# Optimization experiments

Hardware: AMD Instinct MI355X
Metric: run time of the kernel (lower is better)

## Reference

```python
import jax, jax.numpy as jnp
import numpy as np

N_EXPERTS = 8
TOP_K = 2
AUX_COEF = 0.01
Z_COEF = 0.001


def setup_inputs() -> dict:
    key = jax.random.key(0)
    ks = jax.random.split(key, 5)
    B, S, D, F, E = 2, 2048, 768, 2048, N_EXPERTS
    std = 0.02
    std_out = std / np.sqrt(2 * 12)  # scale_init_by_depth, n_layers=12
    return {
        "x": jax.random.normal(ks[0], (B, S, D), jnp.float32),
        "router_w": jax.random.normal(ks[1], (D, E), jnp.float32) * std,
        "w1": jax.random.normal(ks[2], (E, D, F), jnp.float32) * std,
        "w2": jax.random.normal(ks[3], (E, F, D), jnp.float32) * std_out,
        "w3": jax.random.normal(ks[4], (E, D, F), jnp.float32) * std,
    }


def reference(x, router_w, w1, w2, w3):
    B, S, D = x.shape
    E = w1.shape[0]
    x_flat = x.reshape(-1, D)                      # [N, D]
    n_tokens = x_flat.shape[0]

    router_logits = x_flat @ router_w               # [N, E]
    probs = jax.nn.softmax(router_logits.astype(jnp.float32), axis=-1)
    topk_w, topk_i = jax.lax.top_k(probs, TOP_K)    # [N, K]
    topk_w = topk_w / jnp.sum(topk_w, axis=-1, keepdims=True)

    # Combine: equivalent to sort/group dispatch + per-expert GEMM + index_add,
    # expressed as a masked per-expert (fixed, small E) dense pass.
    out = jnp.zeros((n_tokens, D), dtype=x.dtype)
    for e in range(E):
        gate = jnp.sum(jnp.where(topk_i == e, topk_w, 0.0), axis=-1)  # [N] f32
        h = jax.nn.silu(x_flat @ w1[e]) * (x_flat @ w3[e])            # [N, F]
        out = out + gate[:, None].astype(x.dtype) * (h @ w2[e])

    # Switch-style load-balancing aux loss + z-loss
    importance = probs.mean(axis=0)                 # [E]
    top1 = topk_i[:, 0]
    load = jnp.zeros((E,), jnp.float32).at[top1].add(1.0) / n_tokens
    aux_loss = E * jnp.sum(importance * load) * AUX_COEF
    z_loss = jnp.mean(router_logits.astype(jnp.float32) ** 2) * Z_COEF

    return out.reshape(B, S, D), aux_loss, z_loss
```

## Files before the change

### kernel.cpp

```cpp
#include <hip/hip_runtime.h>
#include <hip/hip_bf16.h>

constexpr int NT = 4096;
constexpr int DD = 768;
constexpr int FF = 2048;
constexpr int NE = 8;
constexpr int MAXROWS = 9216;
constexpr int MAXMT128 = 72;
constexpr int MAXMT256 = 40;
constexpr int NKT1 = DD / 64;

constexpr int IDX_CNTA   = 0;
constexpr int IDX_CNTT1  = 8;
constexpr int IDX_CUR    = 16;
constexpr int IDX_IMP    = 24;
constexpr int IDX_ZSUM   = 32;
constexpr int IDX_NTILES = 33;
constexpr int IDX_OFF    = 34;
constexpr int IDX_EXPT   = 48;
constexpr int IDX_N256   = 120;
constexpr int IDX_E256   = 128;
constexpr int IDX_B256   = 168;
constexpr int IDX_L256   = 208;

constexpr size_t OFF_META   = 0;
constexpr size_t OFF_TKE    = 1024;
constexpr size_t OFF_GATE   = OFF_TKE    + (size_t)NT*2*4;
constexpr size_t OFF_ROWOF  = OFF_GATE   + (size_t)NT*2*4;
constexpr size_t OFF_TOKROW = OFF_ROWOF  + (size_t)NT*2*4;
constexpr size_t OFF_XG     = 136192;
constexpr size_t OFF_W1T    = OFF_XG  + (size_t)MAXROWS*DD*2;
constexpr size_t OFF_W3T    = OFF_W1T + (size_t)NE*FF*DD*2;
constexpr size_t OFF_W2T    = OFF_W3T + (size_t)NE*FF*DD*2;
constexpr size_t OFF_H      = OFF_W2T + (size_t)NE*FF*DD*2;
constexpr size_t OFF_OP     = OFF_H   + (size_t)MAXROWS*FF*2;

typedef float f32x4 __attribute__((ext_vector_type(4)));
typedef __bf16 bf16x8v __attribute__((ext_vector_type(8)));
typedef unsigned short u16x8 __attribute__((ext_vector_type(8)));

__device__ inline unsigned short f2bf_bits(float f) {
  __bf16 h = (__bf16)f;
  return *(unsigned short*)&h;
}
__device__ inline float bf2f(unsigned short u) {
  unsigned v = (unsigned)u << 16;
  return *(float*)&v;
}

__device__ __forceinline__ void glds16(const void* g, void* l) {
  __builtin_amdgcn_global_load_lds(
      (const __attribute__((address_space(1))) unsigned int*)g,
      (__attribute__((address_space(3))) unsigned int*)l, 16, 0, 0);
}

constexpr int RB = 128;
__global__ __launch_bounds__(256) void router_kernel(const float* __restrict__ x,
    const float* __restrict__ rw, int* __restrict__ meta,
    int* __restrict__ tke, float* __restrict__ gateArr) {
  __shared__ float s_imp[NE];
  __shared__ float s_z;
  __shared__ int s_cnt1[NE], s_cnta[NE];
  if (threadIdx.x < NE) { s_imp[threadIdx.x] = 0.f; s_cnt1[threadIdx.x] = 0; s_cnta[threadIdx.x] = 0; }
  if (threadIdx.x == 0) s_z = 0.f;
  __syncthreads();

  const int wave = threadIdx.x >> 6, lane = threadIdx.x & 63;
  float impacc[NE];
  #pragma unroll
  for (int e = 0; e < NE; ++e) impacc[e] = 0.f;
  float zacc = 0.f;

  for (int t = blockIdx.x * 4 + wave; t < NT; t += RB * 4) {
    float acc[NE];
    #pragma unroll
    for (int e = 0; e < NE; ++e) acc[e] = 0.f;
    const float* xr = x + (size_t)t * DD;
    for (int i = lane; i < DD; i += 64) {
      float xv = xr[i];
      const float* r = rw + i * NE;
      #pragma unroll
      for (int e = 0; e < NE; ++e) acc[e] += xv * r[e];
    }
    #pragma unroll
    for (int off = 32; off > 0; off >>= 1) {
      #pragma unroll
      for (int e = 0; e < NE; ++e) acc[e] += __shfl_xor(acc[e], off);
    }
    float mx = acc[0];
    #pragma unroll
    for (int e = 1; e < NE; ++e) mx = fmaxf(mx, acc[e]);
    float p[NE]; float s = 0.f;
    #pragma unroll
    for (int e = 0; e < NE; ++e) { p[e] = __expf(acc[e] - mx); s += p[e]; }
    float inv = 1.f / s;
    #pragma unroll
    for (int e = 0; e < NE; ++e) p[e] *= inv;
    int e0 = 0; float p0 = p[0];
    #pragma unroll
    for (int e = 1; e < NE; ++e) if (p[e] > p0) { p0 = p[e]; e0 = e; }
    int e1 = -1; float p1 = -1.f;
    #pragma unroll
    for (int e = 0; e < NE; ++e) if (e != e0 && p[e] > p1) { p1 = p[e]; e1 = e; }
    if (lane == 0) {
      #pragma unroll
      for (int e = 0; e < NE; ++e) { impacc[e] += p[e]; zacc += acc[e] * acc[e]; }
      atomicAdd(&s_cnt1[e0], 1);
      atomicAdd(&s_cnta[e0], 1);
      atomicAdd(&s_cnta[e1], 1);
      float gs = 1.f / (p0 + p1);
      tke[t*2]   = e0; tke[t*2+1] = e1;
      gateArr[t*2] = p0 * gs; gateArr[t*2+1] = p1 * gs;
    }
  }
  if (lane == 0) {
    #pragma unroll
    for (int e = 0; e < NE; ++e) atomicAdd(&s_imp[e], impacc[e]);
    atomicAdd(&s_z, zacc);
  }
  __syncthreads();
  float* fmeta = (float*)meta;
  if (threadIdx.x < NE) {
    atomicAdd(&fmeta[IDX_IMP + threadIdx.x], s_imp[threadIdx.x]);
    atomicAdd(&meta[IDX_CNTT1 + threadIdx.x], s_cnt1[threadIdx.x]);
    atomicAdd(&meta[IDX_CNTA + threadIdx.x], s_cnta[threadIdx.x]);
  }
  if (threadIdx.x == NE) atomicAdd(&fmeta[IDX_ZSUM], s_z);
}

__global__ __launch_bounds__(128) void scan_kernel(int* __restrict__ meta,
                                                   float* __restrict__ out_tail) {
  __shared__ int s_off[NE + 1];
  __shared__ int s_nt[NE];
  __shared__ float s_aux;
  const int t = threadIdx.x;
  if (t < NE) s_nt[t] = (meta[IDX_CNTA + t] + 127) >> 7;
  __syncthreads();
  if (t == 0) {
    int off = 0;
    for (int e = 0; e < NE; ++e) { s_off[e] = off; off += s_nt[e]; }
    s_off[NE] = off;
  }
  __syncthreads();
  const int ntiles = s_off[NE];
  if (t < NE) meta[IDX_OFF + t] = s_off[t] << 7;
  if (t == NE) { meta[IDX_OFF + NE] = ntiles << 7; meta[IDX_NTILES] = ntiles; }
  if (t < ntiles) {
    int e = 0;
    while (t >= s_off[e + 1]) e++;
    meta[IDX_EXPT + t] = e;
  }
  if (t == 0) {
    int n2t = 0;
    for (int e = 0; e < NE; ++e) {
      const int base = s_off[e] << 7;
      const int lim  = base + (s_nt[e] << 7);
      const int n2 = (s_nt[e] + 1) >> 1;
      for (int i = 0; i < n2; ++i) {
        meta[IDX_E256 + n2t] = e;
        meta[IDX_B256 + n2t] = base + (i << 8);
        meta[IDX_L256 + n2t] = lim;
        ++n2t;
      }
    }
    meta[IDX_N256] = n2t;
  }
  float* fmeta = (float*)meta;
  float pl = 0.f;
  if (t < NE)
    pl = (fmeta[IDX_IMP + t] / (float)NT) * ((float)meta[IDX_CNTT1 + t] / (float)NT);
  if (t < 64) {
    #pragma unroll
    for (int off = 4; off > 0; off >>= 1) pl += __shfl_xor(pl, off);
    if (t == 0) s_aux = pl;
  }
  __syncthreads();
  if (t == 0) {
    out_tail[0] = (float)NE * s_aux * 0.01f;
    out_tail[1] = fmeta[IDX_ZSUM] / (float)(NT * NE) * 0.001f;
  }
}

__global__ __launch_bounds__(256) void scatter_kernel(const int* __restrict__ tke,
    int* __restrict__ meta, int* __restrict__ rowof, int* __restrict__ tokrow) {
  __shared__ int s_cnt[NE], s_base[NE];
  const int t = blockIdx.x * 256 + threadIdx.x;
  if (threadIdx.x < NE) s_cnt[threadIdx.x] = 0;
  __syncthreads();
  const int e0 = tke[t*2], e1 = tke[t*2 + 1];
  const int l0 = atomicAdd(&s_cnt[e0], 1);
  const int l1 = atomicAdd(&s_cnt[e1], 1);
  __syncthreads();
  if (threadIdx.x < NE)
    s_base[threadIdx.x] = atomicAdd(&meta[IDX_CUR + threadIdx.x], s_cnt[threadIdx.x]);
  __syncthreads();
  const int r0 = meta[IDX_OFF + e0] + s_base[e0] + l0;
  const int r1 = meta[IDX_OFF + e1] + s_base[e1] + l1;
  rowof[t*2]     = r0;
  rowof[t*2 + 1] = r1;
  tokrow[r0] = t;
  tokrow[r1] = t;
}

__global__ __launch_bounds__(192) void gather_kernel(const float* __restrict__ x,
    const int* __restrict__ tokrow, const int* __restrict__ meta,
    __bf16* __restrict__ Xg) {
  const int row = blockIdx.x;
  if (row >= meta[IDX_OFF + NE]) return;
  const int tok = tokrow[row];
  ushort4* dst = (ushort4*)(Xg + (size_t)row * DD);
  const int i = threadIdx.x;
  ushort4 o;
  if (tok >= 0) {
    float4 v = ((const float4*)(x + (size_t)tok * DD))[i];
    o.x = f2bf_bits(v.x); o.y = f2bf_bits(v.y);
    o.z = f2bf_bits(v.z); o.w = f2bf_bits(v.w);
  } else {
    o.x = o.y = o.z = o.w = 0;
  }
  dst[i] = o;
}

constexpr int TS = 68;
__global__ __launch_bounds__(256) void transpose_cvt_all(
    const float* __restrict__ w1, const float* __restrict__ w3,
    const float* __restrict__ w2, __bf16* __restrict__ W1t,
    __bf16* __restrict__ W3t, __bf16* __restrict__ W2t) {
  const int z = blockIdx.z, which = z >> 3, e = z & 7;
  const float* src; __bf16* dst; int R, C, rt, ct;
  if (which == 0)      { src = w1; dst = W1t; R = DD; C = FF; rt = blockIdx.y; ct = blockIdx.x; }
  else if (which == 1) { src = w3; dst = W3t; R = DD; C = FF; rt = blockIdx.y; ct = blockIdx.x; }
  else                 { src = w2; dst = W2t; R = FF; C = DD; rt = blockIdx.x; ct = blockIdx.y; }
  src += (size_t)e * DD * FF; dst += (size_t)e * DD * FF;
  const int r0 = rt * 64, c0 = ct * 64;
  __shared__ __align__(16) __bf16 tile[64 * TS];
  const int t = threadIdx.x;
  #pragma unroll
  for (int i = 0; i < 4; ++i) {
    int idx = t + i * 256; int r = idx >> 4, q = idx & 15;
    float4 v = *(const float4*)&src[(size_t)(r0 + r) * C + c0 + q * 4];
    ushort4 o;
    o.x = f2bf_bits(v.x); o.y = f2bf_bits(v.y);
    o.z = f2bf_bits(v.z); o.w = f2bf_bits(v.w);
    *(ushort4*)&tile[r * TS + q * 4] = o;
  }
  __syncthreads();
  #pragma unroll
  for (int i = 0; i < 2; ++i) {
    int idx = t + i * 256; int c = idx >> 3, seg = idx & 7;
    u16x8 o;
    #pragma unroll
    for (int k = 0; k < 8; ++k)
      o[k] = *(unsigned short*)&tile[(seg * 8 + k) * TS + c];
    *(u16x8*)&dst[(size_t)(c0 + c) * R + r0 + seg * 8] = o;
  }
}

__global__ __launch_bounds__(512, 2) void gemm1_kernel(
    const __bf16* __restrict__ Xg, const __bf16* __restrict__ W1t,
    const __bf16* __restrict__ W3t, __bf16* __restrict__ Hb,
    const int* __restrict__ meta) {
  const int mt = blockIdx.y;
  if (mt >= meta[IDX_N256]) return;
  const int e      = meta[IDX_E256 + mt];
  const int m0     = meta[IDX_B256 + mt];
  const int rowlim = meta[IDX_L256 + mt];
  const int n0 = blockIdx.x * 128;

  __shared__ __align__(16) __bf16 As[2][256 * 64];
  __shared__ __align__(16) __bf16 Bs[2][256 * 64];

  const int t = threadIdx.x, lane = t & 63, wid = t >> 6;
  const int wm = wid >> 2, wn = wid & 3;
  const int lane15 = lane & 15, g = lane >> 4;

  const __bf16* __restrict__ W1e = W1t + (size_t)e * FF * DD;
  const __bf16* __restrict__ W3e = W3t + (size_t)e * FF * DD;

  const int aBase = (wm * 128 + lane15) * 64;
  const int bBase = (wn * 64 + lane15) * 64;
  const int c0 = ((g    ) ^ (lane & 7)) * 8;
  const int c1 = ((4 + g) ^ (lane & 7)) * 8;

  const f32x4 zero = {0.f, 0.f, 0.f, 0.f};
  f32x4 acc[8][4];
  #pragma unroll
  for (int i = 0; i < 8; ++i)
    #pragma unroll
    for (int j = 0; j < 4; ++j) acc[i][j] = zero;

  __bf16 *Ac = &As[0][0], *An = &As[1][0];
  __bf16 *Bc = &Bs[0][0], *Bn = &Bs[1][0];

  auto stage_a = [&](__bf16* dstBuf, int h, int kt) {
    if (kt >= NKT1) return;
    #pragma unroll
    for (int j = 0; j < 2; ++j) {
      const int o  = j * 512 + t;
      const int r  = o >> 3;
      const int cl = (o & 7) ^ (r & 7);
      int gr = m0 + h * 128 + r;
      if (gr >= MAXROWS) gr = 0;
      glds16(Xg + (size_t)gr * DD + kt * 64 + cl * 8,
             dstBuf + (size_t)(h * 1024 + j * 512 + wid * 64) * 8);
    }
  };
  auto stage_b = [&](__bf16* dstBuf, int h, int kt) {
    if (kt >= NKT1) return;
    #pragma unroll
    for (int j = 0; j < 2; ++j) {
      const int o  = j * 512 + t;
      const int r  = o >> 3;
      const int br = h * 128 + r;
      const int cl = (o & 7) ^ (r & 7);
      const __bf16* wsrc = (br & 16) ? W3e : W1e;
      const int fcol = n0 + ((br >> 5) << 4) + (br & 15);
      glds16(wsrc + (size_t)fcol * DD + kt * 64 + cl * 8,
             dstBuf + (size_t)(h * 1024 + j * 512 + wid * 64) * 8);
    }
  };

  stage_a(Ac, 0, 0);
  stage_a(Ac, 1, 0);
  stage_b(Bc, 0, 0);
  stage_b(Bc, 1, 0);
  stage_a(An, 0, 1);
  stage_a(An, 1, 1);
  asm volatile("s_waitcnt vmcnt(4)" ::: "memory");
  __builtin_amdgcn_s_barrier();

  bf16x8v af[8], ag[8], bfr[4], bgr[4];

  for (int k = 0; k < NKT1; ++k) {
    #pragma unroll
    for (int i = 0; i < 4; ++i) {
      af[i*2+0] = *(const bf16x8v*)&Ac[aBase + i*1024 + c0];
      af[i*2+1] = *(const bf16x8v*)&Ac[aBase + i*1024 + c1];
    }
    #pragma unroll
    for (int j = 0; j < 2; ++j) {
      bfr[j*2+0] = *(const bf16x8v*)&Bc[bBase + j*1024 + c0];
      bfr[j*2+1] = *(const bf16x8v*)&Bc[bBase + j*1024 + c1];
    }
    stage_b(Bn, 0, k + 1);
    __builtin_amdgcn_s_barrier();
    asm volatile("s_waitcnt lgkmcnt(0)" ::: "memory");
    __builtin_amdgcn_s_setprio(1);
    #pragma unroll
    for (int i = 0; i < 4; ++i)
      #pragma unroll
      for (int j = 0; j < 2; ++j) {
        acc[i][j] = __builtin_amdgcn_mfma_f32_16x16x32_bf16(af[i*2+0], bfr[j*2+0], acc[i][j], 0, 0, 0);
        acc[i][j] = __builtin_amdgcn_mfma_f32_16x16x32_bf16(af[i*2+1], bfr[j*2+1], acc[i][j], 0, 0, 0);
      }
    __builtin_amdgcn_s_setprio(0);
    __builtin_amdgcn_s_barrier();

    #pragma unroll
    for (int i = 0; i < 4; ++i) {
      ag[i*2+0] = *(const bf16x8v*)&Ac[aBase + (4+i)*1024 + c0];
      ag[i*2+1] = *(const bf16x8v*)&Ac[aBase + (4+i)*1024 + c1];
    }
    stage_b(Bn, 1, k + 1);
    __builtin_amdgcn_s_barrier();
    asm volatile("s_waitcnt lgkmcnt(0)" ::: "memory");
    __builtin_amdgcn_s_setprio(1);
    #pragma unroll
    for (int i = 0; i < 4; ++i)
      #pragma unroll
      for (int j = 0; j < 2; ++j) {
        acc[4+i][j] = __builtin_amdgcn_mfma_f32_16x16x32_bf16(ag[i*2+0], bfr[j*2+0], acc[4+i][j], 0, 0, 0);
        acc[4+i][j] = __builtin_amdgcn_mfma_f32_16x16x32_bf16(ag[i*2+1], bfr[j*2+1], acc[4+i][j], 0, 0, 0);
      }
    __builtin_amdgcn_s_setprio(0);
    __builtin_amdgcn_s_barrier();

    #pragma unroll
    for (int j = 0; j < 2; ++j) {
      bgr[j*2+0] = *(const bf16x8v*)&Bc[bBase + (2+j)*1024 + c0];
      bgr[j*2+1] = *(const bf16x8v*)&Bc[bBase + (2+j)*1024 + c1];
    }
    stage_a(Ac, 0, k + 2);
    __builtin_amdgcn_s_barrier();
    asm volatile("s_waitcnt lgkmcnt(0)" ::: "memory");
    __builtin_amdgcn_s_setprio(1);
    #pragma unroll
    for (int i = 0; i < 4; ++i)
      #pragma unroll
      for (int j = 0; j < 2; ++j) {
        acc[i][2+j] = __builtin_amdgcn_mfma_f32_16x16x32_bf16(af[i*2+0], bgr[j*2+0], acc[i][2+j], 0, 0, 0);
        acc[i][2+j] = __builtin_amdgcn_mfma_f32_16x16x32_bf16(af[i*2+1], bgr[j*2+1], acc[i][2+j], 0, 0, 0);
      }
    __builtin_amdgcn_s_setprio(0);
    __builtin_amdgcn_s_barrier();

    stage_a(Ac, 1, k + 2);
    __builtin_amdgcn_s_barrier();
    __builtin_amdgcn_s_setprio(1);
    #pragma unroll
    for (int i = 0; i < 4; ++i)
      #pragma unroll
      for (int j = 0; j < 2; ++j) {
        acc[4+i][2+j] = __builtin_amdgcn_mfma_f32_16x16x32_bf16(ag[i*2+0], bgr[j*2+0], acc[4+i][2+j], 0, 0, 0);
        acc[4+i][2+j] = __builtin_amdgcn_mfma_f32_16x16x32_bf16(ag[i*2+1], bgr[j*2+1], acc[4+i][2+j], 0, 0, 0);
      }
    __builtin_amdgcn_s_setprio(0);
    if (k < NKT1 - 2) { asm volatile("s_waitcnt vmcnt(4)" ::: "memory"); }
    else              { asm volatile("s_waitcnt vmcnt(0)" ::: "memory"); }
    __builtin_amdgcn_s_barrier();

    __bf16* tp;
    tp = Ac; Ac = An; An = tp;
    tp = Bc; Bc = Bn; Bn = tp;
  }

  #pragma unroll
  for (int i = 0; i < 8; ++i) {
    const int grow = m0 + wm * 128 + i * 16 + (lane >> 4) * 4;
    #pragma unroll
    for (int p = 0; p < 2; ++p) {
      const int col = n0 + (wn * 2 + p) * 16 + lane15;
      const f32x4 v1 = acc[i][2*p], v3 = acc[i][2*p + 1];
      #pragma unroll
      for (int r = 0; r < 4; ++r) {
        if (grow + r < rowlim) {
          float h = v1[r] / (1.f + __expf(-v1[r])) * v3[r];
          Hb[(size_t)(grow + r) * FF + col] = (__bf16)h;
        }
      }
    }
  }
}

__global__ __launch_bounds__(256) void gemm2_kernel(const __bf16* __restrict__ Hb,
    const __bf16* __restrict__ W2t, __bf16* __restrict__ OP,
    const int* __restrict__ meta) {
  const int mt = blockIdx.y;
  if (mt >= meta[IDX_NTILES]) return;
  const int e = meta[IDX_EXPT + mt];
  const int n0 = blockIdx.x * 128;
  const int m0 = mt * 128;
  __shared__ __align__(16) __bf16 As[128*32], Bs[128*32];
  const int t = threadIdx.x, wave = t >> 6, lane = t & 63;
  const int wm = wave & 1, wn = wave >> 1;
  const __bf16* w2e = W2t + (size_t)e * DD * FF;
  const f32x4 zero = {0.f, 0.f, 0.f, 0.f};
  f32x4 acc[4][4];
  #pragma unroll
  for (int i = 0; i < 4; ++i)
    #pragma unroll
    for (int j = 0; j < 4; ++j) acc[i][j] = zero;

  const __bf16* gA = Hb  + (size_t)(m0 + 32*wave + (lane >> 2)) * FF + (lane & 3) * 8;
  const __bf16* gB = w2e + (size_t)(n0 + 32*wave + (lane >> 2)) * FF + (lane & 3) * 8;
  __bf16* lA0 = &As[(32*wave     ) * 32];
  __bf16* lA1 = &As[(32*wave + 16) * 32];
  __bf16* lB0 = &Bs[(32*wave     ) * 32];
  __bf16* lB1 = &Bs[(32*wave + 16) * 32];

  for (int k0 = 0; k0 < FF; k0 += 32) {
    glds16(gA + k0,          lA0);
    glds16(gA + k0 + 16*FF,  lA1);
    glds16(gB + k0,          lB0);
    glds16(gB + k0 + 16*FF,  lB1);
    __syncthreads();
    bf16x8v a[4], b[4];
    #pragma unroll
    for (int i = 0; i < 4; ++i) {
      a[i] = *(const bf16x8v*)&As[(64*wm + 16*i + (lane & 15))*32 + (lane >> 4)*8];
      b[i] = *(const bf16x8v*)&Bs[(64*wn + 16*i + (lane & 15))*32 + (lane >> 4)*8];
    }
    #pragma unroll
    for (int i = 0; i < 4; ++i)
      #pragma unroll
      for (int j = 0; j < 4; ++j)
        acc[i][j] = __builtin_amdgcn_mfma_f32_16x16x32_bf16(a[i], b[j], acc[i][j], 0, 0, 0);
    __syncthreads();
  }
  #pragma unroll
  for (int i = 0; i < 4; ++i) {
    const int rowb = m0 + 64*wm + 16*i + (lane >> 4)*4;
    #pragma unroll
    for (int j = 0; j < 4; ++j) {
      const int col = n0 + 64*wn + 16*j + (lane & 15);
      #pragma unroll
      for (int r = 0; r < 4; ++r)
        OP[(size_t)(rowb + r)*DD + col] = (__bf16)acc[i][j][r];
    }
  }
}

__global__ __launch_bounds__(192) void combine_kernel(const __bf16* __restrict__ OP,
    const int* __restrict__ rowof, const float* __restrict__ gateArr,
    float* __restrict__ out) {
  const int t = blockIdx.x;
  const int r0 = rowof[t*2], r1 = rowof[t*2 + 1];
  const float g0 = gateArr[t*2], g1 = gateArr[t*2 + 1];
  const ushort4* p0 = (const ushort4*)(OP + (size_t)r0 * DD);
  const ushort4* p1 = (const ushort4*)(OP + (size_t)r1 * DD);
  const int i = threadIdx.x;
  ushort4 a = p0[i], b = p1[i];
  float4 o;
  o.x = g0 * bf2f(a.x) + g1 * bf2f(b.x);
  o.y = g0 * bf2f(a.y) + g1 * bf2f(b.y);
  o.z = g0 * bf2f(a.z) + g1 * bf2f(b.z);
  o.w = g0 * bf2f(a.w) + g1 * bf2f(b.w);
  ((float4*)(out + (size_t)t * DD))[i] = o;
}

extern "C" void kernel_launch(void* const* d_in, const int* in_sizes, int n_in,
                              void* d_out, int out_size, void* d_ws, size_t ws_size,
                              hipStream_t stream) {
  const float* x  = (const float*)d_in[0];
  const float* rw = (const float*)d_in[1];
  const float* w1 = (const float*)d_in[2];
  const float* w2 = (const float*)d_in[3];
  const float* w3 = (const float*)d_in[4];
  float* out = (float*)d_out;

  char* ws = (char*)d_ws;
  int*    meta   = (int*)(ws + OFF_META);
  int*    tke    = (int*)(ws + OFF_TKE);
  float*  gateA  = (float*)(ws + OFF_GATE);
  int*    rowof  = (int*)(ws + OFF_ROWOF);
  int*    tokrow = (int*)(ws + OFF_TOKROW);
  __bf16* Xg     = (__bf16*)(ws + OFF_XG);
  __bf16* W1t    = (__bf16*)(ws + OFF_W1T);
  __bf16* W3t    = (__bf16*)(ws + OFF_W3T);
  __bf16* W2t    = (__bf16*)(ws + OFF_W2T);
  __bf16* Hb     = (__bf16*)(ws + OFF_H);
  __bf16* OP     = (__bf16*)(ws + OFF_OP);

  hipMemsetAsync(ws + OFF_META, 0, 1024, stream);
  hipMemsetAsync(ws + OFF_TOKROW, 0xFF, (size_t)MAXROWS * 4, stream);

  transpose_cvt_all<<<dim3(32, 12, 24), 256, 0, stream>>>(w1, w3, w2, W1t, W3t, W2t);

  router_kernel<<<RB, 256, 0, stream>>>(x, rw, meta, tke, gateA);
  scan_kernel<<<1, 128, 0, stream>>>(meta, out + (size_t)NT * DD);
  scatter_kernel<<<NT/256, 256, 0, stream>>>(tke, meta, rowof, tokrow);
  gather_kernel<<<MAXROWS, 192, 0, stream>>>(x, tokrow, meta, Xg);

  gemm1_kernel<<<dim3(FF/128, MAXMT256), 512, 0, stream>>>(Xg, W1t, W3t, Hb, meta);
  gemm2_kernel<<<dim3(DD/128, MAXMT128), 256, 0, stream>>>(Hb, W2t, OP, meta);
  combine_kernel<<<NT, 192, 0, stream>>>(OP, rowof, gateA, out);
}
```

Before: 382.8 us.

## Remap gemm1 workgroups and prefetch both operands two K-steps ahead

Replaces the 2D grid index with a swizzled linear workgroup id so that consecutive workgroups are spread across M-tiles in a chosen order, intended to improve L2 reuse of expert weights. The B operand is now double-buffered two K-tiles ahead like A, with all B fragments loaded to registers at the start of each step. Global source pointers are precomputed once instead of recomputed per stage, which cuts per-stage address arithmetic. The swizzle hardcodes 80 and 16 column tiles, so the grid shape must match, and it adds register pressure from 8 B fragments plus extra pointers.

```diff
diff --git a/kernel.cpp b/kernel.cpp
--- a/kernel.cpp
+++ b/kernel.cpp
@@ -260,12 +260,14 @@
     const __bf16* __restrict__ Xg, const __bf16* __restrict__ W1t,
     const __bf16* __restrict__ W3t, __bf16* __restrict__ Hb,
     const int* __restrict__ meta) {
-  const int mt = blockIdx.y;
+  const int wgRaw = blockIdx.x + (int)gridDim.x * blockIdx.y;
+  const int wg = (wgRaw & 7) * 80 + (wgRaw >> 3);
+  const int mt = wg >> 4;
+  const int n0 = (wg & 15) * 128;
   if (mt >= meta[IDX_N256]) return;
   const int e      = meta[IDX_E256 + mt];
   const int m0     = meta[IDX_B256 + mt];
   const int rowlim = meta[IDX_L256 + mt];
-  const int n0 = blockIdx.x * 128;
 
   __shared__ __align__(16) __bf16 As[2][256 * 64];
   __shared__ __align__(16) __bf16 Bs[2][256 * 64];
@@ -282,6 +284,36 @@
   const int c0 = ((g    ) ^ (lane & 7)) * 8;
   const int c1 = ((4 + g) ^ (lane & 7)) * 8;
 
+  const int o0v = t, o1v = 512 + t;
+  const int r0v = o0v >> 3, r1v = o1v >> 3;
+  const int cl0 = (o0v & 7) ^ (r0v & 7), cl1 = (o1v & 7) ^ (r1v & 7);
+  int gA00 = m0 + r0v;        if (gA00 >= MAXROWS) gA00 = 0;
+  int gA01 = m0 + r1v;        if (gA01 >= MAXROWS) gA01 = 0;
+  int gA10 = m0 + 128 + r0v;  if (gA10 >= MAXROWS) gA10 = 0;
+  int gA11 = m0 + 128 + r1v;  if (gA11 >= MAXROWS) gA11 = 0;
+  const __bf16* aS00 = Xg + (size_t)gA00 * DD + cl0 * 8;
+  const __bf16* aS01 = Xg + (size_t)gA01 * DD + cl1 * 8;
+  const __bf16* aS10 = Xg + (size_t)gA10 * DD + cl0 * 8;
+  const __bf16* aS11 = Xg + (size_t)gA11 * DD + cl1 * 8;
+  const int fc0 = n0 + ((r0v >> 5) << 4) + (r0v & 15);
+  const int fc1 = n0 + ((r1v >> 5) << 4) + (r1v & 15);
+  const __bf16* bW0 = (r0v & 16) ? W3e : W1e;
+  const __bf16* bW1 = (r1v & 16) ? W3e : W1e;
+  const __bf16* bS00 = bW0 + (size_t)fc0 * DD + cl0 * 8;
+  const __bf16* bS01 = bW1 + (size_t)fc1 * DD + cl1 * 8;
+  const __bf16* bS10 = bW0 + (size_t)(fc0 + 64) * DD + cl0 * 8;
+  const __bf16* bS11 = bW1 + (size_t)(fc1 + 64) * DD + cl1 * 8;
+  const int L00 = (       wid * 64) * 8;
+  const int L01 = ( 512 + wid * 64) * 8;
+  const int L10 = (1024 + wid * 64) * 8;
+  const int L11 = (1536 + wid * 64) * 8;
+
+  auto st2 = [&](__bf16* dstBuf, int kt, const __bf16* s0, const __bf16* s1,
+                 int d0, int d1) {
+    glds16(s0 + (size_t)kt * 64, dstBuf + d0);
+    glds16(s1 + (size_t)kt * 64, dstBuf + d1);
+  };
+
   const f32x4 zero = {0.f, 0.f, 0.f, 0.f};
   f32x4 acc[8][4];
   #pragma unroll
@@ -292,57 +324,27 @@
   __bf16 *Ac = &As[0][0], *An = &As[1][0];
   __bf16 *Bc = &Bs[0][0], *Bn = &Bs[1][0];
 
-  auto stage_a = [&](__bf16* dstBuf, int h, int kt) {
-    if (kt >= NKT1) return;
-    #pragma unroll
-    for (int j = 0; j < 2; ++j) {
-      const int o  = j * 512 + t;
-      const int r  = o >> 3;
-      const int cl = (o & 7) ^ (r & 7);
-      int gr = m0 + h * 128 + r;
-      if (gr >= MAXROWS) gr = 0;
-      glds16(Xg + (size_t)gr * DD + kt * 64 + cl * 8,
-             dstBuf + (size_t)(h * 1024 + j * 512 + wid * 64) * 8);
-    }
-  };
-  auto stage_b = [&](__bf16* dstBuf, int h, int kt) {
-    if (kt >= NKT1) return;
-    #pragma unroll
-    for (int j = 0; j < 2; ++j) {
-      const int o  = j * 512 + t;
-      const int r  = o >> 3;
-      const int br = h * 128 + r;
-      const int cl = (o & 7) ^ (r & 7);
-      const __bf16* wsrc = (br & 16) ? W3e : W1e;
-      const int fcol = n0 + ((br >> 5) << 4) + (br & 15);
-      glds16(wsrc + (size_t)fcol * DD + kt * 64 + cl * 8,
-             dstBuf + (size_t)(h * 1024 + j * 512 + wid * 64) * 8);
-    }
-  };
-
-  stage_a(Ac, 0, 0);
-  stage_a(Ac, 1, 0);
-  stage_b(Bc, 0, 0);
-  stage_b(Bc, 1, 0);
-  stage_a(An, 0, 1);
-  stage_a(An, 1, 1);
-  asm volatile("s_waitcnt vmcnt(4)" ::: "memory");
+  st2(Ac, 0, aS00, aS01, L00, L01); st2(Ac, 0, aS10, aS11, L10, L11);
+  st2(Bc, 0, bS00, bS01, L00, L01); st2(Bc, 0, bS10, bS11, L10, L11);
+  st2(An, 1, aS00, aS01, L00, L01); st2(An, 1, aS10, aS11, L10, L11);
+  st2(Bn, 1, bS00, bS01, L00, L01); st2(Bn, 1, bS10, bS11, L10, L11);
+  asm volatile("s_waitcnt vmcnt(8)" ::: "memory");
   __builtin_amdgcn_s_barrier();
 
-  bf16x8v af[8], ag[8], bfr[4], bgr[4];
+  bf16x8v af[8], ag[8], bf[8];
 
   for (int k = 0; k < NKT1; ++k) {
+    const bool k2ok = (k < NKT1 - 2);
     #pragma unroll
     for (int i = 0; i < 4; ++i) {
       af[i*2+0] = *(const bf16x8v*)&Ac[aBase + i*1024 + c0];
       af[i*2+1] = *(const bf16x8v*)&Ac[aBase + i*1024 + c1];
     }
     #pragma unroll
-    for (int j = 0; j < 2; ++j) {
-      bfr[j*2+0] = *(const bf16x8v*)&Bc[bBase + j*1024 + c0];
-      bfr[j*2+1] = *(const bf16x8v*)&Bc[bBase + j*1024 + c1];
-    }
-    stage_b(Bn, 0, k + 1);
+    for (int j = 0; j < 4; ++j) {
+      bf[j*2+0] = *(const bf16x8v*)&Bc[bBase + j*1024 + c0];
+      bf[j*2+1] = *(const bf16x8v*)&Bc[bBase + j*1024 + c1];
+    }
     __builtin_amdgcn_s_barrier();
     asm volatile("s_waitcnt lgkmcnt(0)" ::: "memory");
     __builtin_amdgcn_s_setprio(1);
@@ -350,8 +352,8 @@
     for (int i = 0; i < 4; ++i)
       #pragma unroll
       for (int j = 0; j < 2; ++j) {
-        acc[i][j] = __builtin_amdgcn_mfma_f32_16x16x32_bf16(af[i*2+0], bfr[j*2+0], acc[i][j], 0, 0, 0);
-        acc[i][j] = __builtin_amdgcn_mfma_f32_16x16x32_bf16(af[i*2+1], bfr[j*2+1], acc[i][j], 0, 0, 0);
+        acc[i][j] = __builtin_amdgcn_mfma_f32_16x16x32_bf16(af[i*2+0], bf[j*2+0], acc[i][j], 0, 0, 0);
+        acc[i][j] = __builtin_amdgcn_mfma_f32_16x16x32_bf16(af[i*2+1], bf[j*2+1], acc[i][j], 0, 0, 0);
       }
     __builtin_amdgcn_s_setprio(0);
     __builtin_amdgcn_s_barrier();
@@ -361,7 +363,7 @@
       ag[i*2+0] = *(const bf16x8v*)&Ac[aBase + (4+i)*1024 + c0];
       ag[i*2+1] = *(const bf16x8v*)&Ac[aBase + (4+i)*1024 + c1];
     }
-    stage_b(Bn, 1, k + 1);
+    if (k2ok) st2(Bc, k + 2, bS00, bS01, L00, L01);
     __builtin_amdgcn_s_barrier();
     asm volatile("s_waitcnt lgkmcnt(0)" ::: "memory");
     __builtin_amdgcn_s_setprio(1);
@@ -369,44 +371,41 @@
     for (int i = 0; i < 4; ++i)
       #pragma unroll
       for (int j = 0; j < 2; ++j) {
-        acc[4+i][j] = __builtin_amdgcn_mfma_f32_16x16x32_bf16(ag[i*2+0], bfr[j*2+0], acc[4+i][j], 0, 0, 0);
-        acc[4+i][j] = __builtin_amdgcn_mfma_f32_16x16x32_bf16(ag[i*2+1], bfr[j*2+1], acc[4+i][j], 0, 0, 0);
+        acc[4+i][j] = __builtin_amdgcn_mfma_f32_16x16x32_bf16(ag[i*2+0], bf[j*2+0], acc[4+i][j], 0, 0, 0);
+        acc[4+i][j] = __builtin_amdgcn_mfma_f32_16x16x32_bf16(ag[i*2+1], bf[j*2+1], acc[4+i][j], 0, 0, 0);
       }
     __builtin_amdgcn_s_setprio(0);
     __builtin_amdgcn_s_barrier();
 
-    #pragma unroll
-    for (int j = 0; j < 2; ++j) {
-      bgr[j*2+0] = *(const bf16x8v*)&Bc[bBase + (2+j)*1024 + c0];
-      bgr[j*2+1] = *(const bf16x8v*)&Bc[bBase + (2+j)*1024 + c1];
-    }
-    stage_a(Ac, 0, k + 2);
-    __builtin_amdgcn_s_barrier();
-    asm volatile("s_waitcnt lgkmcnt(0)" ::: "memory");
+    if (k2ok) {
+      st2(Ac, k + 2, aS00, aS01, L00, L01);
+      st2(Bc, k + 2, bS10, bS11, L10, L11);
+    }
+    __builtin_amdgcn_s_barrier();
     __builtin_amdgcn_s_setprio(1);
     #pragma unroll
     for (int i = 0; i < 4; ++i)
       #pragma unroll
       for (int j = 0; j < 2; ++j) {
-        acc[i][2+j] = __builtin_amdgcn_mfma_f32_16x16x32_bf16(af[i*2+0], bgr[j*2+0], acc[i][2+j], 0, 0, 0);
-        acc[i][2+j] = __builtin_amdgcn_mfma_f32_16x16x32_bf16(af[i*2+1], bgr[j*2+1], acc[i][2+j], 0, 0, 0);
+        acc[i][2+j] = __builtin_amdgcn_mfma_f32_16x16x32_bf16(af[i*2+0], bf[(2+j)*2+0], acc[i][2+j], 0, 0, 0);
+        acc[i][2+j] = __builtin_amdgcn_mfma_f32_16x16x32_bf16(af[i*2+1], bf[(2+j)*2+1], acc[i][2+j], 0, 0, 0);
       }
     __builtin_amdgcn_s_setprio(0);
     __builtin_amdgcn_s_barrier();
 
-    stage_a(Ac, 1, k + 2);
+    if (k2ok) st2(Ac, k + 2, aS10, aS11, L10, L11);
     __builtin_amdgcn_s_barrier();
     __builtin_amdgcn_s_setprio(1);
     #pragma unroll
     for (int i = 0; i < 4; ++i)
       #pragma unroll
       for (int j = 0; j < 2; ++j) {
-        acc[4+i][2+j] = __builtin_amdgcn_mfma_f32_16x16x32_bf16(ag[i*2+0], bgr[j*2+0], acc[4+i][2+j], 0, 0, 0);
-        acc[4+i][2+j] = __builtin_amdgcn_mfma_f32_16x16x32_bf16(ag[i*2+1], bgr[j*2+1], acc[4+i][2+j], 0, 0, 0);
+        acc[4+i][2+j] = __builtin_amdgcn_mfma_f32_16x16x32_bf16(ag[i*2+0], bf[(2+j)*2+0], acc[4+i][2+j], 0, 0, 0);
+        acc[4+i][2+j] = __builtin_amdgcn_mfma_f32_16x16x32_bf16(ag[i*2+1], bf[(2+j)*2+1], acc[4+i][2+j], 0, 0, 0);
       }
     __builtin_amdgcn_s_setprio(0);
-    if (k < NKT1 - 2) { asm volatile("s_waitcnt vmcnt(4)" ::: "memory"); }
-    else              { asm volatile("s_waitcnt vmcnt(0)" ::: "memory"); }
+    if (k2ok)               { asm volatile("s_waitcnt vmcnt(8)" ::: "memory"); }
+    else if (k == NKT1 - 2) { asm volatile("s_waitcnt vmcnt(0)" ::: "memory"); }
     __builtin_amdgcn_s_barrier();
 
     __bf16* tp;
```

Result: slower. 393.1 us (+2.7%).
